# Performance work log

Measured on AMD Instinct MI355X. Metric: run time of the kernel, lower is better.

Reference implementation:

```python
import jax, jax.numpy as jnp
import numpy as np

TEMPERATURE = 0.1
B, D, A = 8192, 256, 4


def setup_inputs() -> dict:
    key = jax.random.key(0)
    k1, k2 = jax.random.split(key)
    # scale by 1/sqrt(D) so dot products are O(1) and exp(sim/T) is finite
    embeddings = jax.random.normal(k1, (B, D), dtype=jnp.float32) / jnp.sqrt(jnp.float32(D))
    labels = jax.random.randint(k2, (B, A), 0, 6, dtype=jnp.int64)
    return {"embeddings": embeddings, "labels": labels}


def reference(embeddings, labels):
    b = embeddings.shape[0]
    # [B, B] similarity scaled by temperature
    sim = jnp.matmul(embeddings, embeddings.T) / TEMPERATURE
    # positive mask: ANY aspect matches (vectorized over aspects), diagonal zeroed
    pos_mask = jnp.any(labels[:, None, :] == labels[None, :, :], axis=-1)
    pos_mask = pos_mask & ~jnp.eye(b, dtype=bool)
    pos_mask = pos_mask.astype(sim.dtype)

    exp_sim = jnp.exp(sim)
    positive_sim = jnp.sum(exp_sim * pos_mask, axis=1)            # [B]
    all_sim = jnp.sum(exp_sim, axis=1) - jnp.diagonal(exp_sim)   # [B]

    valid = positive_sim > 0
    pos_safe = jnp.where(valid, positive_sim, 1.0)
    all_safe = jnp.where(valid, all_sim, 1.0)
    row_loss = jnp.where(valid, -jnp.log(pos_safe / (all_safe + 1e-8)), 0.0)

    num_pos = jnp.sum(valid.astype(sim.dtype))
    loss = jnp.where(num_pos > 0, jnp.sum(row_loss) / jnp.maximum(num_pos, 1.0), 0.0)
    return loss
```

## Files before the change

kernel.cpp:

```cpp
#include <hip/hip_runtime.h>
#include <stdint.h>

typedef short short8 __attribute__((ext_vector_type(8)));
typedef float f32x4 __attribute__((ext_vector_type(4)));
typedef float f32x2 __attribute__((ext_vector_type(2)));
typedef long lng2 __attribute__((ext_vector_type(2)));

#define B_TOTAL 8192
#define DDIM 256
#define BM 256
#define BN 64
#define NSPLIT 16
#define COLS_PER (B_TOTAL / NSPLIT)
#define ITERS (COLS_PER / BN)
#define NBLOCKS ((B_TOTAL / BM) * NSPLIT)
#define SCALE_HALF 3.79828546f
#define LN2F 0.6931471805599453f

typedef __attribute__((address_space(3))) char lds_char;
typedef __attribute__((address_space(1))) const char gbl_char;

__global__ __launch_bounds__(256) void prep_all(
    const float* __restrict__ E, const int* __restrict__ lab,
    unsigned char* __restrict__ Eb8, unsigned int* __restrict__ plab,
    float* __restrict__ posAll) {
  const int t = blockIdx.x * 256 + threadIdx.x;
  const float4* s4 = (const float4*)E + (size_t)t * 2;
  float4 v0 = s4[0], v1 = s4[1];
  unsigned int d0 = (unsigned int)__builtin_amdgcn_cvt_pk_fp8_f32(
      v0.x * SCALE_HALF, v0.y * SCALE_HALF, 0, false);
  d0 = (unsigned int)__builtin_amdgcn_cvt_pk_fp8_f32(
      v0.z * SCALE_HALF, v0.w * SCALE_HALF, (int)d0, true);
  unsigned int d1 = (unsigned int)__builtin_amdgcn_cvt_pk_fp8_f32(
      v1.x * SCALE_HALF, v1.y * SCALE_HALF, 0, false);
  d1 = (unsigned int)__builtin_amdgcn_cvt_pk_fp8_f32(
      v1.z * SCALE_HALF, v1.w * SCALE_HALF, (int)d1, true);
  const int row = t >> 5, j = t & 31;
  unsigned char* orow = Eb8 + (size_t)row * DDIM + ((j & 3) * 64 + (j >> 2) * 8);
  *(unsigned long long*)orow =
      (unsigned long long)d0 | ((unsigned long long)d1 << 32);
  if (t < B_TOTAL) {
    int4 l = ((const int4*)lab)[t];
    plab[t] = (1u << ((unsigned)l.x & 31u))
            | (1u << (((unsigned)l.y & 31u) + 6u))
            | (1u << (((unsigned)l.z & 31u) + 12u))
            | (1u << (((unsigned)l.w & 31u) + 18u));
  }
  if (t < 2 * B_TOTAL) posAll[t] = 0.0f;
}

struct __align__(16) SMem {
  char btile[2][BN * DDIM];
  unsigned int plab_all[COLS_PER];
};

template <int DIAG>
__device__ __forceinline__ void epi_n(
    const f32x4 (&acc)[2], int n, int colbase, int itBN, int l15,
    const unsigned int (&pi)[2][4], const int (&irow)[2][4],
    const unsigned int* __restrict__ plab_all,
    f32x2 (&pos2)[2][2], f32x2 (&all2)[2][2]) {
  const int j = colbase + n * 16 + l15;
  const unsigned int hj = plab_all[itBN + n * 16 + l15];
#pragma unroll
  for (int m = 0; m < 2; ++m) {
    float e[4];
#pragma unroll
    for (int q = 0; q < 4; ++q) {
      float v = __builtin_amdgcn_exp2f(acc[m][q]);
      if (DIAG) { if (j == irow[m][q]) v = 0.0f; }
      e[q] = v;
    }
    f32x2 p01 = { (pi[m][0] & hj) ? e[0] : 0.0f, (pi[m][1] & hj) ? e[1] : 0.0f };
    f32x2 p23 = { (pi[m][2] & hj) ? e[2] : 0.0f, (pi[m][3] & hj) ? e[3] : 0.0f };
    all2[m][0] += (f32x2){e[0], e[1]};
    all2[m][1] += (f32x2){e[2], e[3]};
    pos2[m][0] += p01;
    pos2[m][1] += p23;
  }
}

template <int DIAG>
__device__ __forceinline__ void iter_body(
    const char* __restrict__ btile, const unsigned int* __restrict__ plab_all,
    const long (&afrag)[2][8], const unsigned int (&pi)[2][4],
    const int (&irow)[2][4], int colbase, int itBN, int l15, int l4,
    f32x2 (&pos2)[2][2], f32x2 (&all2)[2][2]) {
  auto kloop = [&](int n, f32x4 (&acc)[2]) {
    acc[0] = (f32x4){0.f, 0.f, 0.f, 0.f};
    acc[1] = (f32x4){0.f, 0.f, 0.f, 0.f};
    const unsigned int rr = (unsigned int)(n * 16 + l15);
#pragma unroll
    for (int kw8 = 0; kw8 < 4; ++kw8) {
      const unsigned int c = (unsigned int)(l4 * 4 + kw8);
      const unsigned int s = c ^ (rr & 7u);
      lng2 b2 = *(const lng2*)(btile + rr * 256u + s * 16u);
      acc[0] = __builtin_amdgcn_mfma_f32_16x16x32_fp8_fp8(
          afrag[0][kw8 * 2], b2[0], acc[0], 0, 0, 0);
      acc[1] = __builtin_amdgcn_mfma_f32_16x16x32_fp8_fp8(
          afrag[1][kw8 * 2], b2[0], acc[1], 0, 0, 0);
      acc[0] = __builtin_amdgcn_mfma_f32_16x16x32_fp8_fp8(
          afrag[0][kw8 * 2 + 1], b2[1], acc[0], 0, 0, 0);
      acc[1] = __builtin_amdgcn_mfma_f32_16x16x32_fp8_fp8(
          afrag[1][kw8 * 2 + 1], b2[1], acc[1], 0, 0, 0);
    }
  };
  f32x4 accA[2], accB[2];
  kloop(0, accA);
  kloop(1, accB);
  epi_n<DIAG>(accA, 0, colbase, itBN, l15, pi, irow, plab_all, pos2, all2);
  kloop(2, accA);
  epi_n<DIAG>(accB, 1, colbase, itBN, l15, pi, irow, plab_all, pos2, all2);
  kloop(3, accB);
  epi_n<DIAG>(accA, 2, colbase, itBN, l15, pi, irow, plab_all, pos2, all2);
  epi_n<DIAG>(accB, 3, colbase, itBN, l15, pi, irow, plab_all, pos2, all2);
}

__global__ __launch_bounds__(512, 2) void main_kernel(
    const unsigned char* __restrict__ Eb8, const unsigned int* __restrict__ plab,
    float* __restrict__ posArr, float* __restrict__ allArr) {
  __shared__ SMem sm;
  const int tid = threadIdx.x;
  const int lane = tid & 63;
  const int wid = tid >> 6;
  const int l15 = lane & 15;
  const int l4 = lane >> 4;
  const int rb = (int)blockIdx.x & 31;
  const int cs = (int)blockIdx.x >> 5;
  const int rowbase = rb * BM;
  const int colstart = cs * COLS_PER;

  auto stage = [&](int bufi, int cb) {
#pragma unroll
    for (int q = 0; q < 2; ++q) {
      const unsigned int base = (unsigned int)q * 8192u + (unsigned int)wid * 1024u;
      const unsigned int L = base + (unsigned int)lane * 16u;
      const unsigned int r = L >> 8;
      const unsigned int s = (L >> 4) & 15u;
      const unsigned int c = s ^ (r & 7u);
      const char* src = (const char*)(Eb8 + (size_t)(cb + (int)r) * DDIM + c * 16);
      char* dst = sm.btile[bufi] + base;
      __builtin_amdgcn_global_load_lds((gbl_char*)src, (lds_char*)dst, 16, 0, 0);
    }
  };

  stage(0, colstart);

  long afrag[2][8];
#pragma unroll
  for (int m = 0; m < 2; ++m) {
    const int row = rowbase + wid * 32 + m * 16 + l15;
    const char* rp = (const char*)Eb8 + (size_t)row * DDIM + l4 * 64;
#pragma unroll
    for (int kw8 = 0; kw8 < 4; ++kw8) {
      lng2 t = *(const lng2*)(rp + kw8 * 16);
      afrag[m][kw8 * 2] = t[0];
      afrag[m][kw8 * 2 + 1] = t[1];
    }
  }

  sm.plab_all[tid] = plab[colstart + tid];

  unsigned int pi[2][4];
  int irow[2][4];
#pragma unroll
  for (int m = 0; m < 2; ++m)
#pragma unroll
    for (int q = 0; q < 4; ++q) {
      const int i = rowbase + wid * 32 + m * 16 + l4 * 4 + q;
      irow[m][q] = i;
      pi[m][q] = plab[i];
    }

  asm volatile("s_waitcnt vmcnt(0) lgkmcnt(0)" ::: "memory");
  __builtin_amdgcn_s_barrier();
  __builtin_amdgcn_sched_barrier(0);

  f32x2 pos2[2][2] = {};
  f32x2 all2[2][2] = {};

  for (int it = 0; it < ITERS; ++it) {
    const int colbase = colstart + it * BN;
    const int cur = it & 1;

    if (it + 1 < ITERS) {
      stage(cur ^ 1, colbase + BN);
      asm volatile("s_waitcnt vmcnt(2)" ::: "memory");
    } else {
      asm volatile("s_waitcnt vmcnt(0)" ::: "memory");
    }
    __builtin_amdgcn_s_barrier();
    __builtin_amdgcn_sched_barrier(0);

    const bool hasDiag = (colbase < rowbase + BM) && (rowbase < colbase + BN);
    if (hasDiag)
      iter_body<1>(sm.btile[cur], sm.plab_all, afrag, pi, irow,
                   colbase, it * BN, l15, l4, pos2, all2);
    else
      iter_body<0>(sm.btile[cur], sm.plab_all, afrag, pi, irow,
                   colbase, it * BN, l15, l4, pos2, all2);

    __builtin_amdgcn_s_barrier();
    __builtin_amdgcn_sched_barrier(0);
  }

#pragma unroll
  for (int m = 0; m < 2; ++m)
#pragma unroll
    for (int q = 0; q < 4; ++q) {
      float p = pos2[m][q >> 1][q & 1], al = all2[m][q >> 1][q & 1];
      p += __shfl_xor(p, 1); p += __shfl_xor(p, 2);
      p += __shfl_xor(p, 4); p += __shfl_xor(p, 8);
      al += __shfl_xor(al, 1); al += __shfl_xor(al, 2);
      al += __shfl_xor(al, 4); al += __shfl_xor(al, 8);
      if (l15 == 0) {
        atomicAdd(&posArr[irow[m][q]], p);
        atomicAdd(&allArr[irow[m][q]], al);
      }
    }
}

__global__ __launch_bounds__(1024) void finalize_kernel(
    const float* __restrict__ posArr, const float* __restrict__ allArr,
    float* __restrict__ out) {
  float ls = 0.f, cnt = 0.f;
#pragma unroll
  for (int k = 0; k < B_TOTAL / 1024; ++k) {
    const int i = threadIdx.x + (k << 10);
    const float p = posArr[i];
    const float a = allArr[i];
    if (p > 0.f) {
      ls += (__builtin_amdgcn_logf(a + 1e-8f) - __builtin_amdgcn_logf(p)) * LN2F;
      cnt += 1.f;
    }
  }
#pragma unroll
  for (int msk = 1; msk < 64; msk <<= 1) {
    ls += __shfl_xor(ls, msk);
    cnt += __shfl_xor(cnt, msk);
  }
  __shared__ float sls[16], scnt[16];
  const int w = threadIdx.x >> 6;
  if ((threadIdx.x & 63) == 0) { sls[w] = ls; scnt[w] = cnt; }
  __syncthreads();
  if (threadIdx.x == 0) {
    float L = 0.f, C = 0.f;
    for (int i = 0; i < 16; ++i) { L += sls[i]; C += scnt[i]; }
    out[0] = (C > 0.f) ? L / fmaxf(C, 1.f) : 0.f;
  }
}

extern "C" void kernel_launch(void* const* d_in, const int* in_sizes, int n_in,
                              void* d_out, int out_size, void* d_ws, size_t ws_size,
                              hipStream_t stream) {
  const float* E = (const float*)d_in[0];
  const int* lab = (const int*)d_in[1];
  float* out = (float*)d_out;
  char* ws = (char*)d_ws;

  unsigned char* Eb8 = (unsigned char*)ws;
  unsigned int* plab = (unsigned int*)(ws + 2u * 1024u * 1024u);
  float* posArr = (float*)(ws + 2u * 1024u * 1024u + 32u * 1024u);
  float* allArr = posArr + B_TOTAL;

  prep_all<<<1024, 256, 0, stream>>>(E, lab, Eb8, plab, posArr);
  main_kernel<<<NBLOCKS, 512, 0, stream>>>(Eb8, plab, posArr, allArr);
  finalize_kernel<<<1, 1024, 0, stream>>>(posArr, allArr, out);
}
```

Baseline: 103.0 us.

## Load B fragments directly from global in MFMA-ready layout, drop LDS staging

The prep kernel now also writes a second copy of the fp8 embeddings, pre-arranged into per-16-column fragment order, so each lane can load its MFMA B operand with contiguous 16-byte global loads. The main kernel drops the double-buffered LDS staging and its barriers, loading B fragments straight into registers with software prefetch across the four sub-tiles. Block size halves to 256 threads with BM=128, doubling the grid. This removes LDS traffic and per-iteration synchronisation, but B tiles are no longer shared through LDS, so L2 and global load traffic rise and register pressure grows.

```diff
diff --git a/kernel.cpp b/kernel.cpp
--- a/kernel.cpp
+++ b/kernel.cpp
@@ -1,14 +1,13 @@
 #include <hip/hip_runtime.h>
 #include <stdint.h>
 
-typedef short short8 __attribute__((ext_vector_type(8)));
 typedef float f32x4 __attribute__((ext_vector_type(4)));
 typedef float f32x2 __attribute__((ext_vector_type(2)));
 typedef long lng2 __attribute__((ext_vector_type(2)));
 
 #define B_TOTAL 8192
 #define DDIM 256
-#define BM 256
+#define BM 128
 #define BN 64
 #define NSPLIT 16
 #define COLS_PER (B_TOTAL / NSPLIT)
@@ -17,13 +16,10 @@
 #define SCALE_HALF 3.79828546f
 #define LN2F 0.6931471805599453f
 
-typedef __attribute__((address_space(3))) char lds_char;
-typedef __attribute__((address_space(1))) const char gbl_char;
-
 __global__ __launch_bounds__(256) void prep_all(
     const float* __restrict__ E, const int* __restrict__ lab,
-    unsigned char* __restrict__ Eb8, unsigned int* __restrict__ plab,
-    float* __restrict__ posAll) {
+    unsigned char* __restrict__ EbA, unsigned char* __restrict__ Bf,
+    unsigned int* __restrict__ plab, float* __restrict__ posAll) {
   const int t = blockIdx.x * 256 + threadIdx.x;
   const float4* s4 = (const float4*)E + (size_t)t * 2;
   float4 v0 = s4[0], v1 = s4[1];
@@ -35,10 +31,16 @@
       v1.x * SCALE_HALF, v1.y * SCALE_HALF, 0, false);
   d1 = (unsigned int)__builtin_amdgcn_cvt_pk_fp8_f32(
       v1.z * SCALE_HALF, v1.w * SCALE_HALF, (int)d1, true);
+  const unsigned long long v8 =
+      (unsigned long long)d0 | ((unsigned long long)d1 << 32);
   const int row = t >> 5, j = t & 31;
-  unsigned char* orow = Eb8 + (size_t)row * DDIM + ((j & 3) * 64 + (j >> 2) * 8);
-  *(unsigned long long*)orow =
-      (unsigned long long)d0 | ((unsigned long long)d1 << 32);
+  *(unsigned long long*)(EbA + (size_t)row * DDIM + ((j & 3) * 64 + (j >> 2) * 8)) = v8;
+  const unsigned int boff = (unsigned int)(row >> 4) * 4096u +
+                            (unsigned int)(j >> 3) * 1024u +
+                            (unsigned int)(j & 3) * 256u +
+                            (unsigned int)(row & 15) * 16u +
+                            (unsigned int)((j >> 2) & 1) * 8u;
+  *(unsigned long long*)(Bf + boff) = v8;
   if (t < B_TOTAL) {
     int4 l = ((const int4*)lab)[t];
     plab[t] = (1u << ((unsigned)l.x & 31u))
@@ -48,11 +50,6 @@
   }
   if (t < 2 * B_TOTAL) posAll[t] = 0.0f;
 }
-
-struct __align__(16) SMem {
-  char btile[2][BN * DDIM];
-  unsigned int plab_all[COLS_PER];
-};
 
 template <int DIAG>
 __device__ __forceinline__ void epi_n(
@@ -82,75 +79,64 @@
 
 template <int DIAG>
 __device__ __forceinline__ void iter_body(
-    const char* __restrict__ btile, const unsigned int* __restrict__ plab_all,
+    const unsigned char* __restrict__ Bf, int ctbase,
+    const unsigned int* __restrict__ plab_all,
     const long (&afrag)[2][8], const unsigned int (&pi)[2][4],
-    const int (&irow)[2][4], int colbase, int itBN, int l15, int l4,
+    const int (&irow)[2][4], int colbase, int itBN, int l15, int lane,
     f32x2 (&pos2)[2][2], f32x2 (&all2)[2][2]) {
-  auto kloop = [&](int n, f32x4 (&acc)[2]) {
+  auto loadB = [&](int n, lng2 (&b)[4]) {
+    const unsigned char* p = Bf + (size_t)(ctbase + n) * 4096 + (unsigned)lane * 16u;
+#pragma unroll
+    for (int kw8 = 0; kw8 < 4; ++kw8) b[kw8] = *(const lng2*)(p + kw8 * 1024);
+  };
+  auto mfmaN = [&](const lng2 (&b)[4], f32x4 (&acc)[2]) {
     acc[0] = (f32x4){0.f, 0.f, 0.f, 0.f};
     acc[1] = (f32x4){0.f, 0.f, 0.f, 0.f};
-    const unsigned int rr = (unsigned int)(n * 16 + l15);
 #pragma unroll
     for (int kw8 = 0; kw8 < 4; ++kw8) {
-      const unsigned int c = (unsigned int)(l4 * 4 + kw8);
-      const unsigned int s = c ^ (rr & 7u);
-      lng2 b2 = *(const lng2*)(btile + rr * 256u + s * 16u);
       acc[0] = __builtin_amdgcn_mfma_f32_16x16x32_fp8_fp8(
-          afrag[0][kw8 * 2], b2[0], acc[0], 0, 0, 0);
+          afrag[0][kw8 * 2], b[kw8][0], acc[0], 0, 0, 0);
       acc[1] = __builtin_amdgcn_mfma_f32_16x16x32_fp8_fp8(
-          afrag[1][kw8 * 2], b2[0], acc[1], 0, 0, 0);
+          afrag[1][kw8 * 2], b[kw8][0], acc[1], 0, 0, 0);
       acc[0] = __builtin_amdgcn_mfma_f32_16x16x32_fp8_fp8(
-          afrag[0][kw8 * 2 + 1], b2[1], acc[0], 0, 0, 0);
+          afrag[0][kw8 * 2 + 1], b[kw8][1], acc[0], 0, 0, 0);
       acc[1] = __builtin_amdgcn_mfma_f32_16x16x32_fp8_fp8(
-          afrag[1][kw8 * 2 + 1], b2[1], acc[1], 0, 0, 0);
+          afrag[1][kw8 * 2 + 1], b[kw8][1], acc[1], 0, 0, 0);
     }
   };
+  lng2 b0[4], b1[4], b2_[4], b3[4];
   f32x4 accA[2], accB[2];
-  kloop(0, accA);
-  kloop(1, accB);
+  loadB(0, b0); loadB(1, b1);
+  mfmaN(b0, accA); loadB(2, b2_);
+  mfmaN(b1, accB);
   epi_n<DIAG>(accA, 0, colbase, itBN, l15, pi, irow, plab_all, pos2, all2);
-  kloop(2, accA);
+  mfmaN(b2_, accA); loadB(3, b3);
   epi_n<DIAG>(accB, 1, colbase, itBN, l15, pi, irow, plab_all, pos2, all2);
-  kloop(3, accB);
+  mfmaN(b3, accB);
   epi_n<DIAG>(accA, 2, colbase, itBN, l15, pi, irow, plab_all, pos2, all2);
   epi_n<DIAG>(accB, 3, colbase, itBN, l15, pi, irow, plab_all, pos2, all2);
 }
 
-__global__ __launch_bounds__(512, 2) void main_kernel(
-    const unsigned char* __restrict__ Eb8, const unsigned int* __restrict__ plab,
+__global__ __launch_bounds__(256, 2) void main_kernel(
+    const unsigned char* __restrict__ EbA, const unsigned char* __restrict__ Bf,
+    const unsigned int* __restrict__ plab,
     float* __restrict__ posArr, float* __restrict__ allArr) {
-  __shared__ SMem sm;
+  __shared__ unsigned int plab_all[COLS_PER];
   const int tid = threadIdx.x;
   const int lane = tid & 63;
   const int wid = tid >> 6;
   const int l15 = lane & 15;
   const int l4 = lane >> 4;
-  const int rb = (int)blockIdx.x & 31;
-  const int cs = (int)blockIdx.x >> 5;
+  const int rb = (int)blockIdx.x & 63;
+  const int cs = (int)blockIdx.x >> 6;
   const int rowbase = rb * BM;
   const int colstart = cs * COLS_PER;
 
-  auto stage = [&](int bufi, int cb) {
-#pragma unroll
-    for (int q = 0; q < 2; ++q) {
-      const unsigned int base = (unsigned int)q * 8192u + (unsigned int)wid * 1024u;
-      const unsigned int L = base + (unsigned int)lane * 16u;
-      const unsigned int r = L >> 8;
-      const unsigned int s = (L >> 4) & 15u;
-      const unsigned int c = s ^ (r & 7u);
-      const char* src = (const char*)(Eb8 + (size_t)(cb + (int)r) * DDIM + c * 16);
-      char* dst = sm.btile[bufi] + base;
-      __builtin_amdgcn_global_load_lds((gbl_char*)src, (lds_char*)dst, 16, 0, 0);
-    }
-  };
-
-  stage(0, colstart);
-
   long afrag[2][8];
 #pragma unroll
   for (int m = 0; m < 2; ++m) {
     const int row = rowbase + wid * 32 + m * 16 + l15;
-    const char* rp = (const char*)Eb8 + (size_t)row * DDIM + l4 * 64;
+    const unsigned char* rp = EbA + (size_t)row * DDIM + l4 * 64;
 #pragma unroll
     for (int kw8 = 0; kw8 < 4; ++kw8) {
       lng2 t = *(const lng2*)(rp + kw8 * 16);
@@ -159,7 +145,8 @@
     }
   }
 
-  sm.plab_all[tid] = plab[colstart + tid];
+  plab_all[tid] = plab[colstart + tid];
+  plab_all[tid + 256] = plab[colstart + 256 + tid];
 
   unsigned int pi[2][4];
   int irow[2][4];
@@ -171,37 +158,21 @@
       irow[m][q] = i;
       pi[m][q] = plab[i];
     }
-
-  asm volatile("s_waitcnt vmcnt(0) lgkmcnt(0)" ::: "memory");
-  __builtin_amdgcn_s_barrier();
-  __builtin_amdgcn_sched_barrier(0);
+  __syncthreads();
 
   f32x2 pos2[2][2] = {};
   f32x2 all2[2][2] = {};
 
   for (int it = 0; it < ITERS; ++it) {
     const int colbase = colstart + it * BN;
-    const int cur = it & 1;
-
-    if (it + 1 < ITERS) {
-      stage(cur ^ 1, colbase + BN);
-      asm volatile("s_waitcnt vmcnt(2)" ::: "memory");
-    } else {
-      asm volatile("s_waitcnt vmcnt(0)" ::: "memory");
-    }
-    __builtin_amdgcn_s_barrier();
-    __builtin_amdgcn_sched_barrier(0);
-
+    const int ctbase = colbase >> 4;
     const bool hasDiag = (colbase < rowbase + BM) && (rowbase < colbase + BN);
     if (hasDiag)
-      iter_body<1>(sm.btile[cur], sm.plab_all, afrag, pi, irow,
-                   colbase, it * BN, l15, l4, pos2, all2);
+      iter_body<1>(Bf, ctbase, plab_all, afrag, pi, irow,
+                   colbase, it * BN, l15, lane, pos2, all2);
     else
-      iter_body<0>(sm.btile[cur], sm.plab_all, afrag, pi, irow,
-                   colbase, it * BN, l15, l4, pos2, all2);
-
-    __builtin_amdgcn_s_barrier();
-    __builtin_amdgcn_sched_barrier(0);
+      iter_body<0>(Bf, ctbase, plab_all, afrag, pi, irow,
+                   colbase, it * BN, l15, lane, pos2, all2);
   }
 
 #pragma unroll
@@ -258,12 +229,13 @@
   float* out = (float*)d_out;
   char* ws = (char*)d_ws;
 
-  unsigned char* Eb8 = (unsigned char*)ws;
-  unsigned int* plab = (unsigned int*)(ws + 2u * 1024u * 1024u);
-  float* posArr = (float*)(ws + 2u * 1024u * 1024u + 32u * 1024u);
+  unsigned char* EbA = (unsigned char*)ws;
+  unsigned char* Bf = (unsigned char*)(ws + 2u * 1024u * 1024u);
+  unsigned int* plab = (unsigned int*)(ws + 4u * 1024u * 1024u);
+  float* posArr = (float*)(ws + 4u * 1024u * 1024u + 32u * 1024u);
   float* allArr = posArr + B_TOTAL;
 
-  prep_all<<<1024, 256, 0, stream>>>(E, lab, Eb8, plab, posArr);
-  main_kernel<<<NBLOCKS, 512, 0, stream>>>(Eb8, plab, posArr, allArr);
+  prep_all<<<1024, 256, 0, stream>>>(E, lab, EbA, Bf, plab, posArr);
+  main_kernel<<<NBLOCKS, 256, 0, stream>>>(EbA, Bf, plab, posArr, allArr);
   finalize_kernel<<<1, 1024, 0, stream>>>(posArr, allArr, out);
 }
```

After: 97.92 us. -4.9%, faster.
